# Performance work log

Hardware: AMD Instinct MI355X
Metric: run time of the kernel (lower is better)

## Reference

```python
import jax, jax.numpy as jnp
import numpy as np

B, S, H, V, T = 32, 64, 512, 32000, 64


def setup_inputs() -> dict:
    key = jax.random.key(0)
    ks = jax.random.split(key, 16)
    sc = 0.02
    return {
        "encoder_outputs": jax.random.normal(ks[0], (B, S, H), jnp.float32),
        "encoder_hidden_state": jax.random.normal(ks[1], (1, B, H), jnp.float32),
        "target_tensor": jax.random.randint(ks[2], (B, T), 0, V),
        "emb": jax.random.normal(ks[3], (V, H), jnp.float32) * sc,
        "Wq": jax.random.normal(ks[4], (H, H), jnp.float32) * sc,
        "bq": jnp.zeros((H,), jnp.float32),
        "Wk": jax.random.normal(ks[5], (H, H), jnp.float32) * sc,
        "bk": jnp.zeros((H,), jnp.float32),
        "Wv": jax.random.normal(ks[6], (1, H), jnp.float32) * sc,
        "bv": jnp.zeros((1,), jnp.float32),
        "W_ih": jax.random.normal(ks[7], (3 * H, 2 * H), jnp.float32) * sc,
        "W_hh": jax.random.normal(ks[8], (3 * H, H), jnp.float32) * sc,
        "b_ih": jnp.zeros((3 * H,), jnp.float32),
        "b_hh": jnp.zeros((3 * H,), jnp.float32),
        "Wo": jax.random.normal(ks[9], (V, H), jnp.float32) * sc,
        "bo": jnp.zeros((V,), jnp.float32),
    }


def _gru_cell(x, h, W_ih, W_hh, b_ih, b_hh):
    # PyTorch GRU cell: gates order (r, z, n)
    gi = x @ W_ih.T + b_ih            # [B, 3H]
    gh = h @ W_hh.T + b_hh            # [B, 3H]
    i_r, i_z, i_n = jnp.split(gi, 3, axis=-1)
    h_r, h_z, h_n = jnp.split(gh, 3, axis=-1)
    r = jax.nn.sigmoid(i_r + h_r)
    z = jax.nn.sigmoid(i_z + h_z)
    n = jnp.tanh(i_n + r * h_n)
    return (1.0 - z) * n + z * h


def reference(encoder_outputs, encoder_hidden_state, target_tensor,
              emb, Wq, bq, Wk, bk, Wv, bv,
              W_ih, W_hh, b_ih, b_hh, Wo, bo):
    # Teacher forcing: input at step i is token 0 (SOS) for i=0, else target[:, i-1]
    batch = encoder_outputs.shape[0]
    sos = jnp.zeros((batch, 1), target_tensor.dtype)
    tokens = jnp.concatenate([sos, target_tensor[:, :-1]], axis=1).T  # [T, B]

    # Precompute key projection once (Bahdanau keys are fixed per sequence)
    k_proj = encoder_outputs @ Wk.T + bk  # [B, S, H]
    h0 = encoder_hidden_state[0]          # [B, H]

    def step(h, tok):
        emb_t = emb[tok]                               # [B, H] (dropout in eval = id)
        q = h @ Wq.T + bq                              # [B, H]
        scores = jnp.einsum('bsh,h->bs', jnp.tanh(q[:, None, :] + k_proj), Wv[0]) + bv[0]
        w = jax.nn.softmax(scores, axis=-1)            # [B, S]
        ctx = jnp.einsum('bs,bsh->bh', w, encoder_outputs)
        x = jnp.concatenate([emb_t, ctx], axis=-1)     # [B, 2H]
        h_new = _gru_cell(x, h, W_ih, W_hh, b_ih, b_hh)
        logits = h_new @ Wo.T + bo                     # [B, V]
        return h_new, (logits, w)

    h_final, (logits, attn) = jax.lax.scan(step, h0, tokens)
    log_probs = jax.nn.log_softmax(jnp.transpose(logits, (1, 0, 2)), axis=-1)  # [B, T, V]
    attentions = jnp.transpose(attn, (1, 0, 2))                                # [B, T, S]
    return log_probs, h_final[None], attentions
```

## Files before the change

### kernel.cpp

```cpp
#include <hip/hip_runtime.h>
#include <hip/hip_bf16.h>

#define B_ 32
#define S_ 64
#define H_ 512
#define V_ 32000
#define T_ 64

typedef __bf16 bf16x8 __attribute__((ext_vector_type(8)));
typedef float f32x4 __attribute__((ext_vector_type(4)));

__device__ __forceinline__ float fast_tanh(float x) {
  float e = __expf(2.0f * x);
  return 1.0f - 2.0f / (e + 1.0f);
}
__device__ __forceinline__ float fast_sigmoid(float x) {
  return 1.0f / (1.0f + __expf(-x));
}
__device__ __forceinline__ int ld_agent(const int* p) {
  return __hip_atomic_load(p, __ATOMIC_RELAXED, __HIP_MEMORY_SCOPE_AGENT);
}
__device__ __forceinline__ void st_agent_f(float* p, float v) {
  __hip_atomic_store(p, v, __ATOMIC_RELAXED, __HIP_MEMORY_SCOPE_AGENT);
}
__device__ __forceinline__ void st_agent_i(int* p, int v) {
  __hip_atomic_store(p, v, __ATOMIC_RELAXED, __HIP_MEMORY_SCOPE_AGENT);
}


__global__ __launch_bounds__(256) void k_emb_gather(const int* __restrict__ target,
    const float* __restrict__ emb, __hip_bfloat16* __restrict__ emb_bf) {
  int row = blockIdx.x;
  int t = row >> 5, b = row & 31;
  int tok = (t == 0) ? 0 : target[b * T_ + t - 1];
  const float* src = emb + (size_t)tok * H_;
  __hip_bfloat16* dst = emb_bf + (size_t)row * H_;
  for (int jj = threadIdx.x; jj < H_; jj += 256) dst[jj] = __float2bfloat16(src[jj]);
}

__global__ __launch_bounds__(256) void k_cvt_dense(const float* __restrict__ src,
    __hip_bfloat16* __restrict__ dst, int n4) {
  int i = blockIdx.x * 256 + threadIdx.x;
  if (i < n4) {
    const float4 v = ((const float4*)src)[i];
    union { __hip_bfloat16 h[4]; uint2 u; } cv;
    cv.h[0] = __float2bfloat16(v.x); cv.h[1] = __float2bfloat16(v.y);
    cv.h[2] = __float2bfloat16(v.z); cv.h[3] = __float2bfloat16(v.w);
    *(uint2*)(dst + (size_t)i * 4) = cv.u;
  }
}

__global__ __launch_bounds__(128) void k_cvt_wihc(const float* __restrict__ W_ih,
    __hip_bfloat16* __restrict__ dst) {
  const int row = blockIdx.x;
  const int c4 = threadIdx.x * 4;
  const float4 v = *(const float4*)(W_ih + (size_t)row * 1024 + 512 + c4);
  union { __hip_bfloat16 h[4]; uint2 u; } cv;
  cv.h[0] = __float2bfloat16(v.x); cv.h[1] = __float2bfloat16(v.y);
  cv.h[2] = __float2bfloat16(v.z); cv.h[3] = __float2bfloat16(v.w);
  *(uint2*)(dst + (size_t)row * 512 + c4) = cv.u;
}

__global__ __launch_bounds__(256) void k_cvt_wqh(const float* __restrict__ Wq,
    const float* __restrict__ W_hh, __hip_bfloat16* __restrict__ wq_bf,
    __hip_bfloat16* __restrict__ whh_bf) {
  const int row = blockIdx.x;
  const int c2 = threadIdx.x * 2;
  const float* src = (row < 512) ? (Wq + (size_t)row * 512)
                                 : (W_hh + (size_t)(row - 512) * 512);
  __hip_bfloat16* dst = (row < 512) ? (wq_bf + (size_t)row * 512)
                                    : (whh_bf + (size_t)(row - 512) * 512);
  const float2 v = *(const float2*)(src + c2);
  union { __hip_bfloat16 h[2]; unsigned u; } cv;
  cv.h[0] = __float2bfloat16(v.x); cv.h[1] = __float2bfloat16(v.y);
  *(unsigned*)(dst + c2) = cv.u;
}

__global__ __launch_bounds__(256) void k_init(const float* __restrict__ ehs,
    float* __restrict__ h_st0, int* __restrict__ flags, float* __restrict__ rowsum) {
  int i = blockIdx.x * 256 + threadIdx.x;
  if (i < B_ * H_) h_st0[i] = ehs[i];
  if (i < 1024)
    __hip_atomic_store(&flags[i], 0, __ATOMIC_RELAXED, __HIP_MEMORY_SCOPE_AGENT);
  if (i < B_ * T_) rowsum[i] = 0.f;
}


__global__ __launch_bounds__(256) void k_gemm_bf16(
    const __hip_bfloat16* __restrict__ A, int lda,
    const float* __restrict__ B, int ldb,
    const float* __restrict__ bias,
    float* __restrict__ C, int ldc, int K) {
  __shared__ float pool[128 * 68];
  __hip_bfloat16* Asub = (__hip_bfloat16*)pool;
  __hip_bfloat16* Bsub = (__hip_bfloat16*)(pool + 2048);
  const int tid = threadIdx.x;
  const int lane = tid & 63, wave = tid >> 6;
  const int wr = wave >> 1, wc = wave & 1;
  const int n0 = blockIdx.x * 128, m0 = blockIdx.y * 128;
  f32x4 acc[4][4];
#pragma unroll
  for (int i = 0; i < 4; ++i)
#pragma unroll
    for (int jj = 0; jj < 4; ++jj) acc[i][jj] = (f32x4){0.f, 0.f, 0.f, 0.f};

  for (int k0 = 0; k0 < K; k0 += 32) {
    uint4 a_v[2];
#pragma unroll
    for (int rr = 0; rr < 2; ++rr) {
      const int seg = tid + rr * 256;
      const int row = seg >> 2, ks8 = (seg & 3) * 8;
      a_v[rr] = *(const uint4*)(A + (size_t)(m0 + row) * lda + k0 + ks8);
    }
    float4 b_v[4];
#pragma unroll
    for (int rr = 0; rr < 4; ++rr) {
      const int idx = tid + rr * 256;
      const int n = idx >> 3, kg = (idx & 7) * 4;
      b_v[rr] = *(const float4*)(B + (size_t)(n0 + n) * ldb + k0 + kg);
    }
    __syncthreads();
#pragma unroll
    for (int rr = 0; rr < 2; ++rr) {
      const int seg = tid + rr * 256;
      *(uint4*)(Asub + seg * 8) = a_v[rr];
    }
#pragma unroll
    for (int rr = 0; rr < 4; ++rr) {
      const int idx = tid + rr * 256;
      const int n = idx >> 3, kg = (idx & 7) * 4;
      union { __hip_bfloat16 h[4]; uint2 u; } cv;
      cv.h[0] = __float2bfloat16(b_v[rr].x);
      cv.h[1] = __float2bfloat16(b_v[rr].y);
      cv.h[2] = __float2bfloat16(b_v[rr].z);
      cv.h[3] = __float2bfloat16(b_v[rr].w);
      *(uint2*)(Bsub + n * 32 + kg) = cv.u;
    }
    __syncthreads();
    bf16x8 af[4], bfr[4];
#pragma unroll
    for (int mi = 0; mi < 4; ++mi)
      af[mi] = *(const bf16x8*)(Asub + (wr * 64 + mi * 16 + (lane & 15)) * 32 + (lane >> 4) * 8);
#pragma unroll
    for (int ni = 0; ni < 4; ++ni)
      bfr[ni] = *(const bf16x8*)(Bsub + (wc * 64 + ni * 16 + (lane & 15)) * 32 + (lane >> 4) * 8);
#pragma unroll
    for (int mi = 0; mi < 4; ++mi)
#pragma unroll
      for (int ni = 0; ni < 4; ++ni)
        acc[mi][ni] = __builtin_amdgcn_mfma_f32_16x16x32_bf16(af[mi], bfr[ni], acc[mi][ni], 0, 0, 0);
  }

  float* Cs = pool;
  const int r4 = (lane >> 4) * 4, cc = lane & 15;
#pragma unroll
  for (int hf = 0; hf < 2; ++hf) {
    __syncthreads();
    if (wc == hf) {
#pragma unroll
      for (int ni = 0; ni < 4; ++ni) {
        const float bb = bias ? bias[n0 + hf * 64 + ni * 16 + cc] : 0.f;
#pragma unroll
        for (int mi = 0; mi < 4; ++mi)
#pragma unroll
          for (int i = 0; i < 4; ++i)
            Cs[(wr * 64 + mi * 16 + r4 + i) * 68 + ni * 16 + cc] = acc[mi][ni][i] + bb;
      }
    }
    __syncthreads();
    const int rowp = tid >> 4, colg = tid & 15;
#pragma unroll
    for (int pass = 0; pass < 8; ++pass) {
      const int row = pass * 16 + rowp;
      const float4 v = *(const float4*)(Cs + row * 68 + colg * 4);
      *(float4*)(C + (size_t)(m0 + row) * ldc + n0 + hf * 64 + colg * 4) = v;
    }
  }
}


__global__ __launch_bounds__(256) void k_recur(
    const __hip_bfloat16* __restrict__ wq_bf, const __hip_bfloat16* __restrict__ whh_bf,
    const float* __restrict__ bq,
    const __hip_bfloat16* __restrict__ kproj_bf,
    const float* __restrict__ Wv, const float* __restrict__ bv,
    const __hip_bfloat16* __restrict__ encT_bf, const float* __restrict__ giemb,
    const float* __restrict__ b_hh,
    float* h_st, float* partial_st, int* flags,
    float* __restrict__ attn_out, __hip_bfloat16* __restrict__ Hall,
    float* __restrict__ hfin) {
  const int tid = threadIdx.x;
  const int bid = blockIdx.x;
  const int b = 4 * (bid & 7) + ((bid >> 3) & 3);
  const int j = bid >> 5;
  int* h_flags  = flags;
  int* st_flags = flags + 512;

  const int rowg = tid >> 3, lane8 = tid & 7;
  const int s_idx = tid >> 2, q4 = tid & 3;
  f32x4 wvr[4];
#pragma unroll
  for (int i = 0; i < 4; ++i)
    wvr[i] = *(const f32x4*)(Wv + j * 64 + q4 * 16 + i * 4);
  float bq2[2];
#pragma unroll
  for (int i = 0; i < 2; ++i) bq2[i] = bq[j * 64 + i * 32 + rowg];
  const float bv0 = bv[0];

  __shared__ float h_s[8 * 68];
  __shared__ float q_s[64];
  __shared__ float gh_s[192];
  __shared__ float ps_s[512];
  __shared__ float w_s[64];
  __shared__ float gic_s[192];

  for (int t = 0; t < T_; ++t) {
    if (tid < 8) {
      while (ld_agent(&h_flags[b * 16 + tid]) < t) __builtin_amdgcn_s_sleep(1);
    }
    __syncthreads();
    asm volatile("" ::: "memory");

    const float* h_t = h_st + (size_t)t * (B_ * H_) + b * H_;
    if (tid < 128) {
      const float4 v = *(const float4*)(h_t + tid * 4);
      const int g = (tid * 4) >> 6, off = (tid * 4) & 63;
      *(float4*)(h_s + g * 68 + off) = v;
    }
    __syncthreads();

    f32x4 hf4[16];
#pragma unroll
    for (int i = 0; i < 16; ++i)
      hf4[i] = *(const f32x4*)(h_s + lane8 * 68 + i * 4);

    auto dotw = [&](const __hip_bfloat16* wrow) -> float {
      const uint4* w8 = (const uint4*)wrow;
      float p = 0.f;
#pragma unroll
      for (int i = 0; i < 8; ++i) {
        const uint4 w = w8[lane8 * 8 + i];
        const f32x4 ha = hf4[2 * i], hb = hf4[2 * i + 1];
        p += __uint_as_float(w.x << 16) * ha[0] + __uint_as_float(w.x & 0xffff0000u) * ha[1];
        p += __uint_as_float(w.y << 16) * ha[2] + __uint_as_float(w.y & 0xffff0000u) * ha[3];
        p += __uint_as_float(w.z << 16) * hb[0] + __uint_as_float(w.z & 0xffff0000u) * hb[1];
        p += __uint_as_float(w.w << 16) * hb[2] + __uint_as_float(w.w & 0xffff0000u) * hb[3];
      }
      p += __shfl_xor(p, 1); p += __shfl_xor(p, 2); p += __shfl_xor(p, 4);
      return p;
    };

#pragma unroll
    for (int i = 0; i < 2; ++i) {
      const float p = dotw(wq_bf + (size_t)(j * 64 + i * 32 + rowg) * 512);
      if (lane8 == 0) q_s[i * 32 + rowg] = p + bq2[i];
    }
    __syncthreads();

    {
      const uint4* kp = (const uint4*)(kproj_bf + ((size_t)(b * S_ + s_idx)) * H_ + j * 64 + q4 * 16);
      const float4* qp = (const float4*)(q_s + q4 * 16);
      float sc = 0.f;
#pragma unroll
      for (int i = 0; i < 2; ++i) {
        const uint4 k = kp[i];
        const float4 qa = qp[2 * i], qb = qp[2 * i + 1];
        const f32x4 va = wvr[2 * i], vb = wvr[2 * i + 1];
        sc += va[0] * fast_tanh(qa.x + __uint_as_float(k.x << 16));
        sc += va[1] * fast_tanh(qa.y + __uint_as_float(k.x & 0xffff0000u));
        sc += va[2] * fast_tanh(qa.z + __uint_as_float(k.y << 16));
        sc += va[3] * fast_tanh(qa.w + __uint_as_float(k.y & 0xffff0000u));
        sc += vb[0] * fast_tanh(qb.x + __uint_as_float(k.z << 16));
        sc += vb[1] * fast_tanh(qb.y + __uint_as_float(k.z & 0xffff0000u));
        sc += vb[2] * fast_tanh(qb.z + __uint_as_float(k.w << 16));
        sc += vb[3] * fast_tanh(qb.w + __uint_as_float(k.w & 0xffff0000u));
      }
      sc += __shfl_xor(sc, 1); sc += __shfl_xor(sc, 2);
      if (q4 == 0)
        st_agent_f(&partial_st[(((size_t)t * B_ + b) * 8 + j) * 64 + s_idx], sc);
    }
    asm volatile("s_waitcnt vmcnt(0)" ::: "memory");
    __syncthreads();
    if (tid == 0)
      st_agent_i(&st_flags[b * 16 + j], t + 1);

#pragma unroll
    for (int i = 0; i < 6; ++i) {
      const int row = (i >> 1) * 512 + j * 64 + (i & 1) * 32 + rowg;
      const float p = dotw(whh_bf + (size_t)row * 512);
      if (lane8 == 0) gh_s[i * 32 + rowg] = p;
    }

    if (tid < 8) {
      while (ld_agent(&st_flags[b * 16 + tid]) < t + 1) __builtin_amdgcn_s_sleep(1);
    }
    __syncthreads();
    asm volatile("" ::: "memory");
    if (tid < 128) {
      const float4 v = *(const float4*)(partial_st + ((size_t)t * B_ + b) * 512 + tid * 4);
      *(float4*)(ps_s + tid * 4) = v;
    }
    __syncthreads();

    if (tid < 64) {
      float sc = bv0;
#pragma unroll
      for (int jj = 0; jj < 8; ++jj) sc += ps_s[jj * 64 + tid];
      float m = sc;
#pragma unroll
      for (int d = 32; d > 0; d >>= 1) m = fmaxf(m, __shfl_xor(m, d));
      const float e = __expf(sc - m);
      float sum = e;
#pragma unroll
      for (int d = 32; d > 0; d >>= 1) sum += __shfl_xor(sum, d);
      const float w = e / sum;
      w_s[tid] = w;
      if (j == (b & 7)) attn_out[((size_t)b * T_ + t) * S_ + tid] = w;
    }
    __syncthreads();

    if (tid < 192) {
      const int g = tid >> 6, dd = tid & 63;
      const int grow = g * H_ + j * 64 + dd;
      const uint4* ep = (const uint4*)(encT_bf + (size_t)grow * 2048 + b * 64);
      const float4* wp4 = (const float4*)w_s;
      float a = 0.f;
#pragma unroll
      for (int i = 0; i < 8; ++i) {
        const uint4 e4 = ep[i];
        const float4 w0 = wp4[2 * i], w1 = wp4[2 * i + 1];
        a += __uint_as_float(e4.x << 16) * w0.x + __uint_as_float(e4.x & 0xffff0000u) * w0.y;
        a += __uint_as_float(e4.y << 16) * w0.z + __uint_as_float(e4.y & 0xffff0000u) * w0.w;
        a += __uint_as_float(e4.z << 16) * w1.x + __uint_as_float(e4.z & 0xffff0000u) * w1.y;
        a += __uint_as_float(e4.w << 16) * w1.z + __uint_as_float(e4.w & 0xffff0000u) * w1.w;
      }
      gic_s[tid] = a;
    }
    __syncthreads();

    if (tid < 64) {
      const int hh = j * 64 + tid;
      const size_t grow = ((size_t)t * B_ + b) * 1536;
      const float ir  = giemb[grow + hh]        + gic_s[tid];
      const float iz  = giemb[grow + 512 + hh]  + gic_s[64 + tid];
      const float in_ = giemb[grow + 1024 + hh] + gic_s[128 + tid];
      const float hr  = gh_s[tid]        + b_hh[hh];
      const float hz  = gh_s[64 + tid]   + b_hh[512 + hh];
      const float hn  = gh_s[128 + tid]  + b_hh[1024 + hh];
      const float rg = fast_sigmoid(ir + hr);
      const float zg = fast_sigmoid(iz + hz);
      const float ng = fast_tanh(in_ + rg * hn);
      const float ho = h_s[j * 68 + tid];
      const float hv = (1.f - zg) * ng + zg * ho;
      st_agent_f(&h_st[(size_t)(t + 1) * (B_ * H_) + b * H_ + hh], hv);
      Hall[((size_t)b * T_ + t) * H_ + hh] = __float2bfloat16(hv);
      if (t == T_ - 1) hfin[b * H_ + hh] = hv;
    }
    asm volatile("s_waitcnt vmcnt(0)" ::: "memory");
    __syncthreads();
    if (tid == 0)
      st_agent_i(&h_flags[b * 16 + j], t + 1);
  }
}


__global__ __launch_bounds__(256) void k_logits(
    const __hip_bfloat16* __restrict__ Hall, const float* __restrict__ Wo,
    const float* __restrict__ bo, float* __restrict__ out0,
    float* __restrict__ rowsum) {
  __shared__ float pool[128 * 68];
  __hip_bfloat16* Asub = (__hip_bfloat16*)pool;
  __hip_bfloat16* Bsub = (__hip_bfloat16*)(pool + 2048);
  const int tid = threadIdx.x;
  const int lane = tid & 63, wave = tid >> 6;
  const int wr = wave >> 1, wc = wave & 1;
  const int flat = blockIdx.x;
  const int nf = (flat & 7) * 500 + (flat >> 3);
  const int m0 = (nf & 15) * 128, n0 = (nf >> 4) * 128;
  f32x4 acc[4][4];
#pragma unroll
  for (int i = 0; i < 4; ++i)
#pragma unroll
    for (int jj = 0; jj < 4; ++jj) acc[i][jj] = (f32x4){0.f, 0.f, 0.f, 0.f};

  for (int k0 = 0; k0 < 512; k0 += 32) {
    uint4 a_v[2];
#pragma unroll
    for (int rr = 0; rr < 2; ++rr) {
      const int seg = tid + rr * 256;
      const int row = seg >> 2, ks8 = (seg & 3) * 8;
      a_v[rr] = *(const uint4*)(Hall + (size_t)(m0 + row) * 512 + k0 + ks8);
    }
    float4 b_v[4];
#pragma unroll
    for (int rr = 0; rr < 4; ++rr) {
      const int idx = tid + rr * 256;
      const int n = idx >> 3, kg = (idx & 7) * 4;
      b_v[rr] = *(const float4*)(Wo + (size_t)(n0 + n) * 512 + k0 + kg);
    }
    __syncthreads();
#pragma unroll
    for (int rr = 0; rr < 2; ++rr) {
      const int seg = tid + rr * 256;
      *(uint4*)(Asub + seg * 8) = a_v[rr];
    }
#pragma unroll
    for (int rr = 0; rr < 4; ++rr) {
      const int idx = tid + rr * 256;
      const int n = idx >> 3, kg = (idx & 7) * 4;
      union { __hip_bfloat16 h[4]; uint2 u; } cv;
      cv.h[0] = __float2bfloat16(b_v[rr].x);
      cv.h[1] = __float2bfloat16(b_v[rr].y);
      cv.h[2] = __float2bfloat16(b_v[rr].z);
      cv.h[3] = __float2bfloat16(b_v[rr].w);
      *(uint2*)(Bsub + n * 32 + kg) = cv.u;
    }
    __syncthreads();
    bf16x8 af[4], bfr[4];
#pragma unroll
    for (int mi = 0; mi < 4; ++mi)
      af[mi] = *(const bf16x8*)(Asub + (wr * 64 + mi * 16 + (lane & 15)) * 32 + (lane >> 4) * 8);
#pragma unroll
    for (int ni = 0; ni < 4; ++ni)
      bfr[ni] = *(const bf16x8*)(Bsub + (wc * 64 + ni * 16 + (lane & 15)) * 32 + (lane >> 4) * 8);
#pragma unroll
    for (int mi = 0; mi < 4; ++mi)
#pragma unroll
      for (int ni = 0; ni < 4; ++ni)
        acc[mi][ni] = __builtin_amdgcn_mfma_f32_16x16x32_bf16(af[mi], bfr[ni], acc[mi][ni], 0, 0, 0);
  }

  float* Cs = pool;
  const int r4 = (lane >> 4) * 4, cc = lane & 15;
#pragma unroll
  for (int hf = 0; hf < 2; ++hf) {
    __syncthreads();
    if (wc == hf) {
#pragma unroll
      for (int ni = 0; ni < 4; ++ni) {
        const float bias = bo[n0 + hf * 64 + ni * 16 + cc];
#pragma unroll
        for (int mi = 0; mi < 4; ++mi)
#pragma unroll
          for (int i = 0; i < 4; ++i)
            Cs[(wr * 64 + mi * 16 + r4 + i) * 68 + ni * 16 + cc] = acc[mi][ni][i] + bias;
      }
    }
    __syncthreads();
    const int rowp = tid >> 4, colg = tid & 15;
#pragma unroll
    for (int pass = 0; pass < 8; ++pass) {
      const int row = pass * 16 + rowp;
      const float4 v = *(const float4*)(Cs + row * 68 + colg * 4);
      *(float4*)(out0 + (size_t)(m0 + row) * V_ + n0 + hf * 64 + colg * 4) = v;
      float e = __expf(v.x) + __expf(v.y) + __expf(v.z) + __expf(v.w);
#pragma unroll
      for (int d = 1; d < 16; d <<= 1) e += __shfl_xor(e, d);
      if (colg == 0) atomicAdd(&rowsum[m0 + row], e);
    }
  }
}


__global__ __launch_bounds__(256) void k_lsm_apply(float* __restrict__ out0,
    const float* __restrict__ rowsum) {
  const int row = blockIdx.x, tid = threadIdx.x;
  const float lse = __logf(rowsum[row]);
  float4* p = (float4*)(out0 + (size_t)row * V_);
  for (int i = tid; i < V_ / 4; i += 256) {
    float4 v = p[i];
    v.x -= lse; v.y -= lse; v.z -= lse; v.w -= lse;
    p[i] = v;
  }
}


extern "C" void kernel_launch(void* const* d_in, const int* in_sizes, int n_in,
                              void* d_out, int out_size, void* d_ws, size_t ws_size,
                              hipStream_t stream) {
  (void)in_sizes; (void)n_in; (void)out_size; (void)ws_size;
  const float* enc  = (const float*)d_in[0];
  const float* ehs  = (const float*)d_in[1];
  const int*   tgt  = (const int*)d_in[2];
  const float* emb  = (const float*)d_in[3];
  const float* Wq   = (const float*)d_in[4];
  const float* bq   = (const float*)d_in[5];
  const float* Wk   = (const float*)d_in[6];
  const float* bk   = (const float*)d_in[7];
  const float* Wv   = (const float*)d_in[8];
  const float* bv   = (const float*)d_in[9];
  const float* W_ih = (const float*)d_in[10];
  const float* W_hh = (const float*)d_in[11];
  const float* b_ih = (const float*)d_in[12];
  const float* b_hh = (const float*)d_in[13];
  const float* Wo   = (const float*)d_in[14];
  const float* bo   = (const float*)d_in[15];

  float* out0 = (float*)d_out;
  float* out1 = out0 + (size_t)B_ * T_ * V_;
  float* out2 = out1 + (size_t)B_ * H_;

  float* kproj    = out0;
  float* giemb    = out0 + 1048576;
  float* encprojT = out0 + 4194304;
  float* h_st     = out0 + 7340032;
  float* partial  = out0 + 8404992;
  __hip_bfloat16* enc_bf   = (__hip_bfloat16*)(out0 + 9453568);
  __hip_bfloat16* emb_bf   = (__hip_bfloat16*)(out0 + 9977856);
  __hip_bfloat16* wihc_bf  = (__hip_bfloat16*)(out0 + 10502144);
  __hip_bfloat16* wq_bf    = (__hip_bfloat16*)(out0 + 10895360);
  __hip_bfloat16* whh_bf   = (__hip_bfloat16*)(out0 + 11026432);
  __hip_bfloat16* kproj_bf = (__hip_bfloat16*)(out0 + 11419648);
  __hip_bfloat16* encT_bf  = (__hip_bfloat16*)(out0 + 11943936);

  __hip_bfloat16* Hall = (__hip_bfloat16*)d_ws;
  int* flags = (int*)((char*)d_ws + (size_t)2 * 1024 * 1024);
  float* rowsum = (float*)((char*)d_ws + (size_t)2 * 1024 * 1024 + 4096);

  k_emb_gather<<<2048, 256, 0, stream>>>(tgt, emb, emb_bf);
  k_cvt_dense<<<1024, 256, 0, stream>>>(enc, enc_bf, 262144);
  k_cvt_wihc<<<1536, 128, 0, stream>>>(W_ih, wihc_bf);
  k_cvt_wqh<<<2048, 256, 0, stream>>>(Wq, W_hh, wq_bf, whh_bf);
  k_init<<<64, 256, 0, stream>>>(ehs, h_st, flags, rowsum);

  k_gemm_bf16<<<dim3(4, 16), 256, 0, stream>>>(enc_bf, 512, Wk, 512, bk, kproj, 512, 512);
  k_gemm_bf16<<<dim3(12, 16), 256, 0, stream>>>(emb_bf, 512, W_ih, 1024, b_ih, giemb, 1536, 512);
  k_gemm_bf16<<<dim3(16, 12), 256, 0, stream>>>(wihc_bf, 512, enc, 512, nullptr, encprojT, 2048, 512);

  k_cvt_dense<<<1024, 256, 0, stream>>>(kproj, kproj_bf, 262144);
  k_cvt_dense<<<3072, 256, 0, stream>>>(encprojT, encT_bf, 786432);

  k_recur<<<256, 256, 0, stream>>>(wq_bf, whh_bf, bq, kproj_bf, Wv, bv, encT_bf,
                                   giemb, b_hh, h_st, partial, flags,
                                   out2, Hall, out1);

  k_logits<<<4000, 256, 0, stream>>>(Hall, Wo, bo, out0, rowsum);
  k_lsm_apply<<<(B_ * T_), 256, 0, stream>>>(out0, rowsum);
}
```

Baseline: 1.254 ms.

## Merge prep kernels, emit bf16 from GEMMs, interleave two batches per recurrent block

Folds the five preparation kernels into one k_prep launch, and has the GEMMs write bf16 directly so the two separate conversion passes go away. The recurrent kernel now runs 128 blocks, each handling two batch rows with interleaved phases, so one batch's dependency wait can overlap the other's work. The logits kernel accumulates its row exp-sums locally before one atomic per row, and spaces rowsum entries 16 floats apart to reduce atomic contention. Risks: twice the serial work per block in the recurrence, and the changed block-to-(batch, slice) mapping has to stay consistent with the flag protocol.

```diff
diff --git a/kernel.cpp b/kernel.cpp
--- a/kernel.cpp
+++ b/kernel.cpp
@@ -28,69 +28,67 @@
 }
 
 
-__global__ __launch_bounds__(256) void k_emb_gather(const int* __restrict__ target,
-    const float* __restrict__ emb, __hip_bfloat16* __restrict__ emb_bf) {
-  int row = blockIdx.x;
-  int t = row >> 5, b = row & 31;
-  int tok = (t == 0) ? 0 : target[b * T_ + t - 1];
-  const float* src = emb + (size_t)tok * H_;
-  __hip_bfloat16* dst = emb_bf + (size_t)row * H_;
-  for (int jj = threadIdx.x; jj < H_; jj += 256) dst[jj] = __float2bfloat16(src[jj]);
-}
-
-__global__ __launch_bounds__(256) void k_cvt_dense(const float* __restrict__ src,
-    __hip_bfloat16* __restrict__ dst, int n4) {
-  int i = blockIdx.x * 256 + threadIdx.x;
-  if (i < n4) {
-    const float4 v = ((const float4*)src)[i];
+__global__ __launch_bounds__(256) void k_prep(
+    const int* __restrict__ tgt, const float* __restrict__ emb,
+    const float* __restrict__ enc, const float* __restrict__ W_ih,
+    const float* __restrict__ Wq, const float* __restrict__ W_hh,
+    const float* __restrict__ ehs,
+    __hip_bfloat16* __restrict__ emb_bf, __hip_bfloat16* __restrict__ enc_bf,
+    __hip_bfloat16* __restrict__ wihc_bf, __hip_bfloat16* __restrict__ wq_bf,
+    __hip_bfloat16* __restrict__ whh_bf,
+    float* __restrict__ h_st0, int* __restrict__ flags,
+    float* __restrict__ rowsum) {
+  const int bid = blockIdx.x, tid = threadIdx.x;
+  if (bid < 2048) {
+    const int t = bid >> 5, b = bid & 31;
+    const int tok = (t == 0) ? 0 : tgt[b * T_ + t - 1];
+    const float* src = emb + (size_t)tok * H_;
+    __hip_bfloat16* dst = emb_bf + (size_t)bid * H_;
+    for (int jj = tid; jj < H_; jj += 256) dst[jj] = __float2bfloat16(src[jj]);
+  } else if (bid < 3072) {
+    const int i = (bid - 2048) * 256 + tid;
+    const float4 v = ((const float4*)enc)[i];
     union { __hip_bfloat16 h[4]; uint2 u; } cv;
     cv.h[0] = __float2bfloat16(v.x); cv.h[1] = __float2bfloat16(v.y);
     cv.h[2] = __float2bfloat16(v.z); cv.h[3] = __float2bfloat16(v.w);
-    *(uint2*)(dst + (size_t)i * 4) = cv.u;
-  }
-}
-
-__global__ __launch_bounds__(128) void k_cvt_wihc(const float* __restrict__ W_ih,
-    __hip_bfloat16* __restrict__ dst) {
-  const int row = blockIdx.x;
-  const int c4 = threadIdx.x * 4;
-  const float4 v = *(const float4*)(W_ih + (size_t)row * 1024 + 512 + c4);
-  union { __hip_bfloat16 h[4]; uint2 u; } cv;
-  cv.h[0] = __float2bfloat16(v.x); cv.h[1] = __float2bfloat16(v.y);
-  cv.h[2] = __float2bfloat16(v.z); cv.h[3] = __float2bfloat16(v.w);
-  *(uint2*)(dst + (size_t)row * 512 + c4) = cv.u;
-}
-
-__global__ __launch_bounds__(256) void k_cvt_wqh(const float* __restrict__ Wq,
-    const float* __restrict__ W_hh, __hip_bfloat16* __restrict__ wq_bf,
-    __hip_bfloat16* __restrict__ whh_bf) {
-  const int row = blockIdx.x;
-  const int c2 = threadIdx.x * 2;
-  const float* src = (row < 512) ? (Wq + (size_t)row * 512)
-                                 : (W_hh + (size_t)(row - 512) * 512);
-  __hip_bfloat16* dst = (row < 512) ? (wq_bf + (size_t)row * 512)
-                                    : (whh_bf + (size_t)(row - 512) * 512);
-  const float2 v = *(const float2*)(src + c2);
-  union { __hip_bfloat16 h[2]; unsigned u; } cv;
-  cv.h[0] = __float2bfloat16(v.x); cv.h[1] = __float2bfloat16(v.y);
-  *(unsigned*)(dst + c2) = cv.u;
-}
-
-__global__ __launch_bounds__(256) void k_init(const float* __restrict__ ehs,
-    float* __restrict__ h_st0, int* __restrict__ flags, float* __restrict__ rowsum) {
-  int i = blockIdx.x * 256 + threadIdx.x;
-  if (i < B_ * H_) h_st0[i] = ehs[i];
-  if (i < 1024)
-    __hip_atomic_store(&flags[i], 0, __ATOMIC_RELAXED, __HIP_MEMORY_SCOPE_AGENT);
-  if (i < B_ * T_) rowsum[i] = 0.f;
-}
-
-
-__global__ __launch_bounds__(256) void k_gemm_bf16(
+    *(uint2*)(enc_bf + (size_t)i * 4) = cv.u;
+  } else if (bid < 4608) {
+    if (tid < 128) {
+      const int row = bid - 3072;
+      const int c4 = tid * 4;
+      const float4 v = *(const float4*)(W_ih + (size_t)row * 1024 + 512 + c4);
+      union { __hip_bfloat16 h[4]; uint2 u; } cv;
+      cv.h[0] = __float2bfloat16(v.x); cv.h[1] = __float2bfloat16(v.y);
+      cv.h[2] = __float2bfloat16(v.z); cv.h[3] = __float2bfloat16(v.w);
+      *(uint2*)(wihc_bf + (size_t)row * 512 + c4) = cv.u;
+    }
+  } else if (bid < 6656) {
+    const int row = bid - 4608;
+    const int c2 = tid * 2;
+    const float* src = (row < 512) ? (Wq + (size_t)row * 512)
+                                   : (W_hh + (size_t)(row - 512) * 512);
+    __hip_bfloat16* dst = (row < 512) ? (wq_bf + (size_t)row * 512)
+                                      : (whh_bf + (size_t)(row - 512) * 512);
+    const float2 v = *(const float2*)(src + c2);
+    union { __hip_bfloat16 h[2]; unsigned u; } cv;
+    cv.h[0] = __float2bfloat16(v.x); cv.h[1] = __float2bfloat16(v.y);
+    *(unsigned*)(dst + c2) = cv.u;
+  } else {
+    const int i = (bid - 6656) * 256 + tid;
+    if (i < 16384) h_st0[i] = ehs[i];
+    else if (i < 17408)
+      __hip_atomic_store(&flags[i - 16384], 0, __ATOMIC_RELAXED, __HIP_MEMORY_SCOPE_AGENT);
+    else if (i < 50176) rowsum[i - 17408] = 0.f;
+  }
+}
+
+
+template <bool BF16OUT>
+__global__ __launch_bounds__(256) void k_gemm(
     const __hip_bfloat16* __restrict__ A, int lda,
     const float* __restrict__ B, int ldb,
     const float* __restrict__ bias,
-    float* __restrict__ C, int ldc, int K) {
+    void* __restrict__ Cv, int ldc, int K) {
   __shared__ float pool[128 * 68];
   __hip_bfloat16* Asub = (__hip_bfloat16*)pool;
   __hip_bfloat16* Bsub = (__hip_bfloat16*)(pool + 2048);
@@ -173,7 +171,14 @@
     for (int pass = 0; pass < 8; ++pass) {
       const int row = pass * 16 + rowp;
       const float4 v = *(const float4*)(Cs + row * 68 + colg * 4);
-      *(float4*)(C + (size_t)(m0 + row) * ldc + n0 + hf * 64 + colg * 4) = v;
+      if constexpr (BF16OUT) {
+        union { __hip_bfloat16 h[4]; uint2 u; } cv;
+        cv.h[0] = __float2bfloat16(v.x); cv.h[1] = __float2bfloat16(v.y);
+        cv.h[2] = __float2bfloat16(v.z); cv.h[3] = __float2bfloat16(v.w);
+        *(uint2*)((__hip_bfloat16*)Cv + (size_t)(m0 + row) * ldc + n0 + hf * 64 + colg * 4) = cv.u;
+      } else {
+        *(float4*)((float*)Cv + (size_t)(m0 + row) * ldc + n0 + hf * 64 + colg * 4) = v;
+      }
     }
   }
 }
@@ -191,8 +196,9 @@
     float* __restrict__ hfin) {
   const int tid = threadIdx.x;
   const int bid = blockIdx.x;
-  const int b = 4 * (bid & 7) + ((bid >> 3) & 3);
-  const int j = bid >> 5;
+  const int c = (bid & 7) + 8 * ((bid >> 6) & 1);
+  const int j = (bid >> 3) & 7;
+  const int b0 = 2 * c, b1 = 2 * c + 1;
   int* h_flags  = flags;
   int* st_flags = flags + 512;
 
@@ -207,32 +213,31 @@
   for (int i = 0; i < 2; ++i) bq2[i] = bq[j * 64 + i * 32 + rowg];
   const float bv0 = bv[0];
 
-  __shared__ float h_s[8 * 68];
+  __shared__ float h_s[2][8 * 68];
+  __shared__ float gh_s[2][192];
   __shared__ float q_s[64];
-  __shared__ float gh_s[192];
   __shared__ float ps_s[512];
   __shared__ float w_s[64];
   __shared__ float gic_s[192];
 
-  for (int t = 0; t < T_; ++t) {
+  auto phase1 = [&](int b, int sel, int t) {
     if (tid < 8) {
       while (ld_agent(&h_flags[b * 16 + tid]) < t) __builtin_amdgcn_s_sleep(1);
     }
     __syncthreads();
     asm volatile("" ::: "memory");
-
     const float* h_t = h_st + (size_t)t * (B_ * H_) + b * H_;
     if (tid < 128) {
       const float4 v = *(const float4*)(h_t + tid * 4);
       const int g = (tid * 4) >> 6, off = (tid * 4) & 63;
-      *(float4*)(h_s + g * 68 + off) = v;
+      *(float4*)(&h_s[sel][g * 68 + off]) = v;
     }
     __syncthreads();
 
     f32x4 hf4[16];
 #pragma unroll
     for (int i = 0; i < 16; ++i)
-      hf4[i] = *(const f32x4*)(h_s + lane8 * 68 + i * 4);
+      hf4[i] = *(const f32x4*)(&h_s[sel][lane8 * 68 + i * 4]);
 
     auto dotw = [&](const __hip_bfloat16* wrow) -> float {
       const uint4* w8 = (const uint4*)wrow;
@@ -288,9 +293,11 @@
     for (int i = 0; i < 6; ++i) {
       const int row = (i >> 1) * 512 + j * 64 + (i & 1) * 32 + rowg;
       const float p = dotw(whh_bf + (size_t)row * 512);
-      if (lane8 == 0) gh_s[i * 32 + rowg] = p;
-    }
-
+      if (lane8 == 0) gh_s[sel][i * 32 + rowg] = p;
+    }
+  };
+
+  auto phase2 = [&](int b, int sel, int t) {
     if (tid < 8) {
       while (ld_agent(&st_flags[b * 16 + tid]) < t + 1) __builtin_amdgcn_s_sleep(1);
     }
@@ -344,13 +351,13 @@
       const float ir  = giemb[grow + hh]        + gic_s[tid];
       const float iz  = giemb[grow + 512 + hh]  + gic_s[64 + tid];
       const float in_ = giemb[grow + 1024 + hh] + gic_s[128 + tid];
-      const float hr  = gh_s[tid]        + b_hh[hh];
-      const float hz  = gh_s[64 + tid]   + b_hh[512 + hh];
-      const float hn  = gh_s[128 + tid]  + b_hh[1024 + hh];
+      const float hr  = gh_s[sel][tid]        + b_hh[hh];
+      const float hz  = gh_s[sel][64 + tid]   + b_hh[512 + hh];
+      const float hn  = gh_s[sel][128 + tid]  + b_hh[1024 + hh];
       const float rg = fast_sigmoid(ir + hr);
       const float zg = fast_sigmoid(iz + hz);
       const float ng = fast_tanh(in_ + rg * hn);
-      const float ho = h_s[j * 68 + tid];
+      const float ho = h_s[sel][j * 68 + tid];
       const float hv = (1.f - zg) * ng + zg * ho;
       st_agent_f(&h_st[(size_t)(t + 1) * (B_ * H_) + b * H_ + hh], hv);
       Hall[((size_t)b * T_ + t) * H_ + hh] = __float2bfloat16(hv);
@@ -360,6 +367,13 @@
     __syncthreads();
     if (tid == 0)
       st_agent_i(&h_flags[b * 16 + j], t + 1);
+  };
+
+  for (int t = 0; t < T_; ++t) {
+    phase1(b0, 0, t);
+    phase1(b1, 1, t);
+    phase2(b0, 0, t);
+    phase2(b1, 1, t);
   }
 }
 
@@ -432,6 +446,8 @@
 
   float* Cs = pool;
   const int r4 = (lane >> 4) * 4, cc = lane & 15;
+  const int rowp = tid >> 4, colg = tid & 15;
+  float es[8] = {0.f, 0.f, 0.f, 0.f, 0.f, 0.f, 0.f, 0.f};
 #pragma unroll
   for (int hf = 0; hf < 2; ++hf) {
     __syncthreads();
@@ -447,17 +463,21 @@
       }
     }
     __syncthreads();
-    const int rowp = tid >> 4, colg = tid & 15;
 #pragma unroll
     for (int pass = 0; pass < 8; ++pass) {
       const int row = pass * 16 + rowp;
       const float4 v = *(const float4*)(Cs + row * 68 + colg * 4);
       *(float4*)(out0 + (size_t)(m0 + row) * V_ + n0 + hf * 64 + colg * 4) = v;
-      float e = __expf(v.x) + __expf(v.y) + __expf(v.z) + __expf(v.w);
-#pragma unroll
-      for (int d = 1; d < 16; d <<= 1) e += __shfl_xor(e, d);
-      if (colg == 0) atomicAdd(&rowsum[m0 + row], e);
-    }
+      es[pass] += __expf(v.x) + __expf(v.y) + __expf(v.z) + __expf(v.w);
+    }
+  }
+#pragma unroll
+  for (int pass = 0; pass < 8; ++pass) {
+    float e = es[pass];
+#pragma unroll
+    for (int d = 1; d < 16; d <<= 1) e += __shfl_xor(e, d);
+    if (colg == 0)
+      atomicAdd(&rowsum[(size_t)(m0 + pass * 16 + rowp) * 16], e);
   }
 }
 
@@ -465,7 +485,7 @@
 __global__ __launch_bounds__(256) void k_lsm_apply(float* __restrict__ out0,
     const float* __restrict__ rowsum) {
   const int row = blockIdx.x, tid = threadIdx.x;
-  const float lse = __logf(rowsum[row]);
+  const float lse = __logf(rowsum[(size_t)row * 16]);
   float4* p = (float4*)(out0 + (size_t)row * V_);
   for (int i = tid; i < V_ / 4; i += 256) {
     float4 v = p[i];
@@ -500,37 +520,30 @@
   float* out1 = out0 + (size_t)B_ * T_ * V_;
   float* out2 = out1 + (size_t)B_ * H_;
 
-  float* kproj    = out0;
-  float* giemb    = out0 + 1048576;
-  float* encprojT = out0 + 4194304;
-  float* h_st     = out0 + 7340032;
-  float* partial  = out0 + 8404992;
-  __hip_bfloat16* enc_bf   = (__hip_bfloat16*)(out0 + 9453568);
-  __hip_bfloat16* emb_bf   = (__hip_bfloat16*)(out0 + 9977856);
-  __hip_bfloat16* wihc_bf  = (__hip_bfloat16*)(out0 + 10502144);
-  __hip_bfloat16* wq_bf    = (__hip_bfloat16*)(out0 + 10895360);
-  __hip_bfloat16* whh_bf   = (__hip_bfloat16*)(out0 + 11026432);
-  __hip_bfloat16* kproj_bf = (__hip_bfloat16*)(out0 + 11419648);
-  __hip_bfloat16* encT_bf  = (__hip_bfloat16*)(out0 + 11943936);
+  float* giemb    = out0;
+  float* h_st     = out0 + 3145728;
+  float* partial  = out0 + 4210688;
+  __hip_bfloat16* enc_bf   = (__hip_bfloat16*)(out0 + 5259264);
+  __hip_bfloat16* emb_bf   = (__hip_bfloat16*)(out0 + 5783552);
+  __hip_bfloat16* wihc_bf  = (__hip_bfloat16*)(out0 + 6307840);
+  __hip_bfloat16* wq_bf    = (__hip_bfloat16*)(out0 + 6701056);
+  __hip_bfloat16* whh_bf   = (__hip_bfloat16*)(out0 + 6832128);
+  __hip_bfloat16* kproj_bf = (__hip_bfloat16*)(out0 + 7225344);
+  __hip_bfloat16* encT_bf  = (__hip_bfloat16*)(out0 + 7749632);
 
   __hip_bfloat16* Hall = (__hip_bfloat16*)d_ws;
   int* flags = (int*)((char*)d_ws + (size_t)2 * 1024 * 1024);
   float* rowsum = (float*)((char*)d_ws + (size_t)2 * 1024 * 1024 + 4096);
 
-  k_emb_gather<<<2048, 256, 0, stream>>>(tgt, emb, emb_bf);
-  k_cvt_dense<<<1024, 256, 0, stream>>>(enc, enc_bf, 262144);
-  k_cvt_wihc<<<1536, 128, 0, stream>>>(W_ih, wihc_bf);
-  k_cvt_wqh<<<2048, 256, 0, stream>>>(Wq, W_hh, wq_bf, whh_bf);
-  k_init<<<64, 256, 0, stream>>>(ehs, h_st, flags, rowsum);
-
-  k_gemm_bf16<<<dim3(4, 16), 256, 0, stream>>>(enc_bf, 512, Wk, 512, bk, kproj, 512, 512);
-  k_gemm_bf16<<<dim3(12, 16), 256, 0, stream>>>(emb_bf, 512, W_ih, 1024, b_ih, giemb, 1536, 512);
-  k_gemm_bf16<<<dim3(16, 12), 256, 0, stream>>>(wihc_bf, 512, enc, 512, nullptr, encprojT, 2048, 512);
-
-  k_cvt_dense<<<1024, 256, 0, stream>>>(kproj, kproj_bf, 262144);
-  k_cvt_dense<<<3072, 256, 0, stream>>>(encprojT, encT_bf, 786432);
-
-  k_recur<<<256, 256, 0, stream>>>(wq_bf, whh_bf, bq, kproj_bf, Wv, bv, encT_bf,
+  k_prep<<<6853, 256, 0, stream>>>(tgt, emb, enc, W_ih, Wq, W_hh, ehs,
+                                   emb_bf, enc_bf, wihc_bf, wq_bf, whh_bf,
+                                   h_st, flags, rowsum);
+
+  k_gemm<true><<<dim3(4, 16), 256, 0, stream>>>(enc_bf, 512, Wk, 512, bk, kproj_bf, 512, 512);
+  k_gemm<false><<<dim3(12, 16), 256, 0, stream>>>(emb_bf, 512, W_ih, 1024, b_ih, giemb, 1536, 512);
+  k_gemm<true><<<dim3(16, 12), 256, 0, stream>>>(wihc_bf, 512, enc, 512, nullptr, encT_bf, 2048, 512);
+
+  k_recur<<<128, 256, 0, stream>>>(wq_bf, whh_bf, bq, kproj_bf, Wv, bv, encT_bf,
                                    giemb, b_hh, h_st, partial, flags,
                                    out2, Hall, out1);
 
```

Result: slower. 1.976 ms (+57.7%).
